# Kernel tuning notes

Hardware: AMD Instinct MI355X
Metric: run time of the kernel (lower is better)

## Reference

```python
import jax, jax.numpy as jnp
import numpy as np

K = 24            # patch_size (window)
D = 4             # dilation
C = 256           # dim
H = 8             # num_heads
N = 500000        # number of octree tokens at this depth (nnum_t)
BATCH_SIZE = 8
BLOCK = K * D
NA = int(np.ceil(N / BLOCK)) * BLOCK   # nnum_a (padded length)
PAD = NA - N
SCALE = (C // H) ** -0.5
MASK_VAL = -1000.0


def setup_inputs() -> dict:
    key = jax.random.key(0)
    k1, k2, k3, k4 = jax.random.split(key, 4)
    data = jax.random.normal(k1, (N, C), jnp.float32)
    qkv_w = jax.random.normal(k2, (3 * C, C), jnp.float32) * 0.02
    qkv_b = jnp.zeros((3 * C,), jnp.float32)
    proj_w = jax.random.normal(k3, (C, C), jnp.float32) * 0.02
    proj_b = jnp.zeros((C,), jnp.float32)
    batch_idx = jnp.sort(jax.random.randint(k4, (N,), 0, BATCH_SIZE, dtype=jnp.int32))
    return {"data": data, "qkv_w": qkv_w, "qkv_b": qkv_b,
            "proj_w": proj_w, "proj_b": proj_b, "batch_idx": batch_idx}


def _dilate_mask(batch_idx):
    # patch_partition of batch ids: pad with fill_value = batch_size
    b = jnp.concatenate([batch_idx, jnp.full((PAD,), BATCH_SIZE, jnp.int32)], axis=0)
    # dilate reshuffle: (-1, K, D) -> transpose -> (-1, K) windows
    b = b.reshape(-1, K, D).transpose(0, 2, 1).reshape(-1, K)
    diff = b[:, :, None] - b[:, None, :]           # [nw, K, K]
    return jnp.where(diff != 0, MASK_VAL, 0.0).astype(jnp.float32)


def reference(data, qkv_w, qkv_b, proj_w, proj_b, batch_idx):
    mask = _dilate_mask(batch_idx)                              # [nw, K, K]
    # patch_partition of features: pad with zeros
    x = jnp.concatenate([data, jnp.zeros((PAD, C), data.dtype)], axis=0)
    # dilation reshuffle: (-1, K, D, C) -> (-1, D, K, C) -> windows [nw, K, C]
    x = x.reshape(-1, K, D, C).transpose(0, 2, 1, 3).reshape(-1, K, C)
    qkv = (x @ qkv_w.T + qkv_b).reshape(-1, K, 3, H, C // H).transpose(2, 0, 3, 1, 4)
    q, k, v = qkv[0] * SCALE, qkv[1], qkv[2]                    # [nw, H, K, hd]
    attn = jnp.einsum('nhqd,nhkd->nhqk', q, k) + mask[:, None]  # [nw, H, K, K]
    attn = jax.nn.softmax(attn, axis=-1)
    out = jnp.einsum('nhqk,nhkd->nhqd', attn, v)
    out = out.transpose(0, 2, 1, 3).reshape(-1, C)              # merge heads
    # reverse dilation reshuffle, drop padding (patch_reverse)
    out = out.reshape(-1, D, K, C).transpose(0, 2, 1, 3).reshape(-1, C)[:N]
    return out @ proj_w.T + proj_b
```

## Files before the change

### kernel.cpp

```cpp
#include <hip/hip_runtime.h>


#define N_TOK 500000
#define NA    500064
#define MP    500096
#define MT    3907
#define MT8   3912
#define CDIM  256
#define KWIN  24
#define NWIN  20836
#define HEADS 8
#define SCALE_F 0.17677669529663689f

typedef __attribute__((ext_vector_type(8))) short bf16x8;
typedef __attribute__((ext_vector_type(4))) float f32x4;

__device__ __forceinline__ unsigned short f2b(float f) {
    unsigned int u = __float_as_uint(f);
    u += 0x7fffu + ((u >> 16) & 1u);
    return (unsigned short)(u >> 16);
}

#define GLOAD_LDS16(gsrc, ldst) \
    __builtin_amdgcn_global_load_lds((const __attribute__((address_space(1))) void*)(gsrc), \
                                     (__attribute__((address_space(3))) void*)(ldst), 16, 0, 0)


__global__ __launch_bounds__(256) void cvt_w_kernel(const float* __restrict__ src,
                                                    unsigned short* __restrict__ dst, int n8) {
    int i = blockIdx.x * 256 + threadIdx.x;
    if (i >= n8) return;
    float4 a = ((const float4*)src)[i * 2];
    float4 b = ((const float4*)src)[i * 2 + 1];
    uint4 o;
    o.x = (unsigned)f2b(a.x) | ((unsigned)f2b(a.y) << 16);
    o.y = (unsigned)f2b(a.z) | ((unsigned)f2b(a.w) << 16);
    o.z = (unsigned)f2b(b.x) | ((unsigned)f2b(b.y) << 16);
    o.w = (unsigned)f2b(b.z) | ((unsigned)f2b(b.w) << 16);
    ((uint4*)dst)[i] = o;
}


__global__ __launch_bounds__(256, 3) void qkv_gemm_kernel(const float* __restrict__ A32,
                                                          const unsigned short* __restrict__ Bt,
                                                          const float* __restrict__ bias,
                                                          unsigned short* __restrict__ out) {
    __shared__ unsigned short ldsA[128 * 64];
    __shared__ unsigned short ldsB[128 * 64];
    const int l = blockIdx.x;
    const int s = l >> 3;
    const int mtile = (l & 7) + 8 * (s / 6);
    const int ntile = s - (s / 6) * 6;
    if (mtile >= MT) return;

    const int tid  = threadIdx.x;
    const int lane = tid & 63;
    const int wv   = tid >> 6;
    const int wr   = wv >> 1, wc = wv & 1;

    f32x4 acc[4][4];
    #pragma unroll
    for (int i = 0; i < 4; ++i)
        #pragma unroll
        for (int j = 0; j < 4; ++j)
            #pragma unroll
            for (int r = 0; r < 4; ++r) acc[i][j][r] = 0.f;

    const char*  bbase = (const char*)(Bt + (size_t)ntile * 128 * CDIM);
    const int lrow8 = lane >> 3;
    const int lcolb_sw = (((lane & 7) ^ lrow8) << 4);
    const int arow  = tid >> 4;
    const int acol  = (tid & 15) * 4;
    const int awz   = (arow & 7) << 4;
    const int growb = mtile * 128;
    const bool full_tile = (growb + 128 <= N_TOK);
    char* ldsA_b = (char*)ldsA;
    const int lrow = lane & 15, lg = lane >> 4;
    const int swzr = (lrow & 7) << 4;

    for (int kt = 0; kt < 4; ++kt) {
        #pragma unroll
        for (int c = 0; c < 4; ++c) {
            int chunk = wv * 4 + c;
            int row = chunk * 8 + lrow8;
            GLOAD_LDS16(bbase + (size_t)row * 512 + kt * 128 + lcolb_sw, &ldsB[chunk * 512]);
        }
        float4 areg[8];
        if (full_tile) {
            #pragma unroll
            for (int i = 0; i < 8; ++i) {
                int row_g = growb + i * 16 + arow;
                areg[i] = *(const float4*)(A32 + (size_t)row_g * CDIM + kt * 64 + acol);
            }
        } else {
            #pragma unroll
            for (int i = 0; i < 8; ++i) {
                int row_g = growb + i * 16 + arow;
                int row_c = row_g < N_TOK ? row_g : (N_TOK - 1);
                areg[i] = *(const float4*)(A32 + (size_t)row_c * CDIM + kt * 64 + acol);
            }
            #pragma unroll
            for (int i = 0; i < 8; ++i)
                if (growb + i * 16 + arow >= N_TOK) areg[i] = make_float4(0.f, 0.f, 0.f, 0.f);
        }
        #pragma unroll
        for (int i = 0; i < 8; ++i) {
            float4 a = areg[i];
            uint2 o;
            o.x = (unsigned)f2b(a.x) | ((unsigned)f2b(a.y) << 16);
            o.y = (unsigned)f2b(a.z) | ((unsigned)f2b(a.w) << 16);
            *(uint2*)(ldsA_b + (i * 16 + arow) * 128 + (((tid & 15) * 8) ^ awz)) = o;
        }
        __syncthreads();
        #pragma unroll
        for (int ks = 0; ks < 2; ++ks) {
            const int kbyte = ks * 64 + lg * 16;
            bf16x8 af[4], bfr[4];
            #pragma unroll
            for (int i = 0; i < 4; ++i) {
                int ra = wr * 64 + i * 16 + lrow;
                int rb = wc * 64 + i * 16 + lrow;
                af[i]  = *(const bf16x8*)(ldsA_b + ra * 128 + (kbyte ^ swzr));
                bfr[i] = *(const bf16x8*)((const char*)ldsB + rb * 128 + (kbyte ^ swzr));
            }
            #pragma unroll
            for (int i = 0; i < 4; ++i)
                #pragma unroll
                for (int j = 0; j < 4; ++j)
                    acc[i][j] = __builtin_amdgcn_mfma_f32_16x16x32_bf16(af[i], bfr[j], acc[i][j], 0, 0, 0);
        }
        __syncthreads();
    }

    #pragma unroll
    for (int i = 0; i < 4; ++i) {
        int row0 = mtile * 128 + wr * 64 + i * 16 + lg * 4;
        #pragma unroll
        for (int j = 0; j < 4; ++j) {
            int col = ntile * 128 + wc * 64 + j * 16 + lrow;
            float bv = bias[col];
            #pragma unroll
            for (int r = 0; r < 4; ++r)
                out[(size_t)(row0 + r) * 768 + col] = f2b(acc[i][j][r] + bv);
        }
    }
}


__global__ __launch_bounds__(512, 2) void attn_proj_kernel(const unsigned short* __restrict__ qkv,
                                                           const int* __restrict__ batch_idx,
                                                           const unsigned short* __restrict__ wproj,
                                                           const float* __restrict__ pbias,
                                                           float* __restrict__ dout) {
    __shared__ unsigned short sP[8][32 * 64];
    __shared__ unsigned short sX[32 * 256];

    const int bid = blockIdx.x;
    const int xcd = bid & 7, sidx = bid >> 3;
    const int qch = NWIN >> 3, rch = NWIN & 7;
    const int w = (xcd < rch ? xcd * (qch + 1) : rch * (qch + 1) + (xcd - rch) * qch) + sidx;

    const int tid  = threadIdx.x;
    const int lane = tid & 63;
    const int h    = tid >> 6;
    const int gw = w >> 2, dd = w & 3;
    const int lrow = lane & 15, lg = lane >> 4;
    const int pbase = gw * 96 + dd;

    bf16x8 Qf[2], Kf[2];
    #pragma unroll
    for (int t = 0; t < 2; ++t) {
        size_t p = (size_t)(pbase + (t * 16 + lrow) * 4);
        const unsigned short* bp = qkv + p * 768 + h * 32 + lg * 8;
        Qf[t] = *(const bf16x8*)bp;
        Kf[t] = *(const bf16x8*)(bp + 256);
    }
    unsigned short v0[8], v1[8];
    #pragma unroll
    for (int j2 = 0; j2 < 8; ++j2) {
        size_t p = (size_t)(pbase + (lg * 8 + j2) * 4);
        const unsigned short* vp = qkv + p * 768 + 512 + h * 32 + lrow;
        v0[j2] = vp[0];
        v1[j2] = vp[16];
    }
    int bq[2];
    #pragma unroll
    for (int j = 0; j < 2; ++j) {
        int r = j * 16 + lrow;
        int p = pbase + r * 4;
        bq[j] = (r < KWIN && p < N_TOK) ? batch_idx[p] : -1;
    }
    int bk[2][4];
    #pragma unroll
    for (int i = 0; i < 2; ++i)
        #pragma unroll
        for (int rr = 0; rr < 4; ++rr) {
            int r = i * 16 + lg * 4 + rr;
            int p = pbase + r * 4;
            bk[i][rr] = (r < KWIN && p < N_TOK) ? batch_idx[p] : -2;
        }

    f32x4 accS[2][2];
    #pragma unroll
    for (int i = 0; i < 2; ++i)
        #pragma unroll
        for (int j = 0; j < 2; ++j)
            #pragma unroll
            for (int r = 0; r < 4; ++r) accS[i][j][r] = 0.f;
    #pragma unroll
    for (int i = 0; i < 2; ++i)
        #pragma unroll
        for (int j = 0; j < 2; ++j)
            accS[i][j] = __builtin_amdgcn_mfma_f32_16x16x32_bf16(Kf[i], Qf[j], accS[i][j], 0, 0, 0);

    float sv[2][2][4];
    float mx[2] = { -3.0e38f, -3.0e38f };
    #pragma unroll
    for (int i = 0; i < 2; ++i)
        #pragma unroll
        for (int j = 0; j < 2; ++j)
            #pragma unroll
            for (int rr = 0; rr < 4; ++rr) {
                float val = (bk[i][rr] == bq[j]) ? accS[i][j][rr] * SCALE_F : -1.0e9f;
                sv[i][j][rr] = val;
                mx[j] = fmaxf(mx[j], val);
            }
    mx[0] = fmaxf(mx[0], __shfl_xor(mx[0], 16)); mx[0] = fmaxf(mx[0], __shfl_xor(mx[0], 32));
    mx[1] = fmaxf(mx[1], __shfl_xor(mx[1], 16)); mx[1] = fmaxf(mx[1], __shfl_xor(mx[1], 32));
    float sm[2] = { 0.f, 0.f };
    #pragma unroll
    for (int i = 0; i < 2; ++i)
        #pragma unroll
        for (int j = 0; j < 2; ++j)
            #pragma unroll
            for (int rr = 0; rr < 4; ++rr) {
                float e = __expf(sv[i][j][rr] - mx[j]);
                sv[i][j][rr] = e;
                sm[j] += e;
            }
    sm[0] += __shfl_xor(sm[0], 16); sm[0] += __shfl_xor(sm[0], 32);
    sm[1] += __shfl_xor(sm[1], 16); sm[1] += __shfl_xor(sm[1], 32);
    float inv[2] = { 1.f / sm[0], 1.f / sm[1] };

    char* pb = (char*)sP[h];
    const int swz = (lrow & 7) << 4;
    #pragma unroll
    for (int j = 0; j < 2; ++j) {
        int q = j * 16 + lrow;
        #pragma unroll
        for (int i = 0; i < 2; ++i) {
            unsigned lo = (unsigned)f2b(sv[i][j][0] * inv[j]) | ((unsigned)f2b(sv[i][j][1] * inv[j]) << 16);
            unsigned hi = (unsigned)f2b(sv[i][j][2] * inv[j]) | ((unsigned)f2b(sv[i][j][3] * inv[j]) << 16);
            *(uint2*)(pb + q * 128 + ((i * 32 + lg * 8) ^ swz)) = make_uint2(lo, hi);
        }
    }
    bf16x8 AP[2];
    #pragma unroll
    for (int jj = 0; jj < 2; ++jj)
        AP[jj] = *(const bf16x8*)(pb + (jj * 16 + lrow) * 128 + ((lg * 16) ^ swz));

    union { bf16x8 v; unsigned short s[8]; } B0, B1;
    #pragma unroll
    for (int j2 = 0; j2 < 8; ++j2) { B0.s[j2] = v0[j2]; B1.s[j2] = v1[j2]; }
    f32x4 accO[2][2];
    #pragma unroll
    for (int i = 0; i < 2; ++i)
        #pragma unroll
        for (int j = 0; j < 2; ++j)
            #pragma unroll
            for (int r = 0; r < 4; ++r) accO[i][j][r] = 0.f;
    #pragma unroll
    for (int jj = 0; jj < 2; ++jj) {
        accO[jj][0] = __builtin_amdgcn_mfma_f32_16x16x32_bf16(AP[jj], B0.v, accO[jj][0], 0, 0, 0);
        accO[jj][1] = __builtin_amdgcn_mfma_f32_16x16x32_bf16(AP[jj], B1.v, accO[jj][1], 0, 0, 0);
    }

    char* xb = (char*)sX;
    #pragma unroll
    for (int jj = 0; jj < 2; ++jj)
        #pragma unroll
        for (int nd = 0; nd < 2; ++nd)
            #pragma unroll
            for (int rr = 0; rr < 4; ++rr) {
                int q = jj * 16 + lg * 4 + rr;
                int c = h * 32 + nd * 16 + lrow;
                *(unsigned short*)(xb + q * 512 + ((c * 2) ^ ((q & 15) << 4))) = f2b(accO[jj][nd][rr]);
            }

    bf16x8 WB[2][8];
    #pragma unroll
    for (int nt = 0; nt < 2; ++nt)
        #pragma unroll
        for (int k8 = 0; k8 < 8; ++k8)
            WB[nt][k8] = *(const bf16x8*)(wproj + (size_t)(h * 32 + nt * 16 + lrow) * 256 + k8 * 32 + lg * 8);

    __syncthreads();

    f32x4 acc2[2][2];
    #pragma unroll
    for (int mt = 0; mt < 2; ++mt)
        #pragma unroll
        for (int nt = 0; nt < 2; ++nt)
            #pragma unroll
            for (int r = 0; r < 4; ++r) acc2[mt][nt][r] = 0.f;
    #pragma unroll
    for (int k8 = 0; k8 < 8; ++k8) {
        bf16x8 aA[2];
        #pragma unroll
        for (int mt = 0; mt < 2; ++mt)
            aA[mt] = *(const bf16x8*)(xb + (mt * 16 + lrow) * 512 + ((k8 * 64 + lg * 16) ^ (lrow << 4)));
        #pragma unroll
        for (int mt = 0; mt < 2; ++mt)
            #pragma unroll
            for (int nt = 0; nt < 2; ++nt)
                acc2[mt][nt] = __builtin_amdgcn_mfma_f32_16x16x32_bf16(aA[mt], WB[nt][k8], acc2[mt][nt], 0, 0, 0);
    }

    #pragma unroll
    for (int nt = 0; nt < 2; ++nt) {
        int n = h * 32 + nt * 16 + lrow;
        float bv = pbias[n];
        #pragma unroll
        for (int mt = 0; mt < 2; ++mt)
            #pragma unroll
            for (int rr = 0; rr < 4; ++rr) {
                int q = mt * 16 + lg * 4 + rr;
                int p = pbase + q * 4;
                if (q < KWIN && p < N_TOK)
                    dout[(size_t)p * CDIM + n] = acc2[mt][nt][rr] + bv;
            }
    }
}


extern "C" void kernel_launch(void* const* d_in, const int* in_sizes, int n_in,
                              void* d_out, int out_size, void* d_ws, size_t ws_size,
                              hipStream_t stream) {
    const float* data    = (const float*)d_in[0];
    const float* qkv_w   = (const float*)d_in[1];
    const float* qkv_b   = (const float*)d_in[2];
    const float* proj_w  = (const float*)d_in[3];
    const float* proj_b  = (const float*)d_in[4];
    const int*   batch_i = (const int*)d_in[5];

    char* ws = (char*)d_ws;
    size_t off = 0;
    unsigned short* qkvB   = (unsigned short*)(ws + off); off += (size_t)MP * 768 * 2;
    unsigned short* wqkvB  = (unsigned short*)(ws + off); off += (size_t)768 * 256 * 2;
    unsigned short* wprojB = (unsigned short*)(ws + off); off += (size_t)256 * 256 * 2;
    if (ws_size < off) return;

    cvt_w_kernel<<<(768 * 256 / 8 + 255) / 256, 256, 0, stream>>>(qkv_w, wqkvB, 768 * 256 / 8);
    cvt_w_kernel<<<(256 * 256 / 8 + 255) / 256, 256, 0, stream>>>(proj_w, wprojB, 256 * 256 / 8);

    qkv_gemm_kernel<<<MT8 * 6, 256, 0, stream>>>(data, wqkvB, qkv_b, qkvB);
    attn_proj_kernel<<<NWIN, 512, 0, stream>>>(qkvB, batch_i, wprojB, proj_b, (float*)d_out);
}
```

Baseline: 1.005 ms.

## Process a full 96-token window group per block with LDS-staged QKV

Measured after the change: 954.9 us. 1.05x faster.

```diff
diff --git a/kernel.cpp b/kernel.cpp
--- a/kernel.cpp
+++ b/kernel.cpp
@@ -6,9 +6,9 @@
 #define MP    500096
 #define MT    3907
 #define MT8   3912
+#define NG    5209
 #define CDIM  256
 #define KWIN  24
-#define NWIN  20836
 #define HEADS 8
 #define SCALE_F 0.17677669529663689f
 
@@ -147,170 +147,199 @@
 }
 
 
-__global__ __launch_bounds__(512, 2) void attn_proj_kernel(const unsigned short* __restrict__ qkv,
+__global__ __launch_bounds__(512, 1) void attn_proj_kernel(const unsigned short* __restrict__ qkv,
                                                            const int* __restrict__ batch_idx,
                                                            const unsigned short* __restrict__ wproj,
                                                            const float* __restrict__ pbias,
                                                            float* __restrict__ dout) {
-    __shared__ unsigned short sP[8][32 * 64];
-    __shared__ unsigned short sX[32 * 256];
-
-    const int bid = blockIdx.x;
-    const int xcd = bid & 7, sidx = bid >> 3;
-    const int qch = NWIN >> 3, rch = NWIN & 7;
-    const int w = (xcd < rch ? xcd * (qch + 1) : rch * (qch + 1) + (xcd - rch) * qch) + sidx;
-
+    __shared__ __align__(16) unsigned char ldsx[162816];
+    const int g    = blockIdx.x;
     const int tid  = threadIdx.x;
     const int lane = tid & 63;
-    const int h    = tid >> 6;
-    const int gw = w >> 2, dd = w & 3;
+    const int wv   = tid >> 6;
     const int lrow = lane & 15, lg = lane >> 4;
-    const int pbase = gw * 96 + dd;
-
-    bf16x8 Qf[2], Kf[2];
-    #pragma unroll
-    for (int t = 0; t < 2; ++t) {
-        size_t p = (size_t)(pbase + (t * 16 + lrow) * 4);
-        const unsigned short* bp = qkv + p * 768 + h * 32 + lg * 8;
-        Qf[t] = *(const bf16x8*)bp;
-        Kf[t] = *(const bf16x8*)(bp + 256);
-    }
-    unsigned short v0[8], v1[8];
-    #pragma unroll
-    for (int j2 = 0; j2 < 8; ++j2) {
-        size_t p = (size_t)(pbase + (lg * 8 + j2) * 4);
-        const unsigned short* vp = qkv + p * 768 + 512 + h * 32 + lrow;
-        v0[j2] = vp[0];
-        v1[j2] = vp[16];
-    }
-    int bq[2];
-    #pragma unroll
-    for (int j = 0; j < 2; ++j) {
-        int r = j * 16 + lrow;
-        int p = pbase + r * 4;
-        bq[j] = (r < KWIN && p < N_TOK) ? batch_idx[p] : -1;
-    }
-    int bk[2][4];
-    #pragma unroll
-    for (int i = 0; i < 2; ++i)
-        #pragma unroll
-        for (int rr = 0; rr < 4; ++rr) {
-            int r = i * 16 + lg * 4 + rr;
-            int p = pbase + r * 4;
-            bk[i][rr] = (r < KWIN && p < N_TOK) ? batch_idx[p] : -2;
-        }
-
-    f32x4 accS[2][2];
-    #pragma unroll
-    for (int i = 0; i < 2; ++i)
-        #pragma unroll
-        for (int j = 0; j < 2; ++j)
-            #pragma unroll
-            for (int r = 0; r < 4; ++r) accS[i][j][r] = 0.f;
-    #pragma unroll
-    for (int i = 0; i < 2; ++i)
-        #pragma unroll
-        for (int j = 0; j < 2; ++j)
-            accS[i][j] = __builtin_amdgcn_mfma_f32_16x16x32_bf16(Kf[i], Qf[j], accS[i][j], 0, 0, 0);
-
-    float sv[2][2][4];
-    float mx[2] = { -3.0e38f, -3.0e38f };
-    #pragma unroll
-    for (int i = 0; i < 2; ++i)
-        #pragma unroll
-        for (int j = 0; j < 2; ++j)
+
+    const char* gbase = (const char*)qkv + (size_t)g * 147456;
+    #pragma unroll
+    for (int c = 0; c < 18; ++c) {
+        int s = c * 512 + tid;
+        int row = s / 96;
+        int c16 = s - row * 96;
+        int srcb = (c16 * 16) ^ (((row >> 2) & 7) << 4);
+        GLOAD_LDS16(gbase + row * 1536 + srcb, ldsx + (size_t)(c * 512 + wv * 64) * 16);
+    }
+    __syncthreads();
+
+    const char* X = (const char*)ldsx;
+    char* sPw = (char*)ldsx + 147456 + wv * 1920;
+    f32x4 accO4[4][2][2];
+
+    #pragma unroll
+    for (int tt = 0; tt < 4; ++tt) {
+        const int task = wv * 4 + tt;
+        const int dd = task >> 3, h = task & 7;
+
+        bf16x8 Qf[2], Kf[2];
+        #pragma unroll
+        for (int t = 0; t < 2; ++t) {
+            int q  = t * 16 + lrow;
+            int rq = (q < KWIN) ? q * 4 + dd : dd;
+            int sz = ((rq >> 2) & 7) << 4;
+            Qf[t] = *(const bf16x8*)(X + rq * 1536 + ((h * 64 + lg * 16) ^ sz));
+            Kf[t] = *(const bf16x8*)(X + rq * 1536 + ((512 + h * 64 + lg * 16) ^ sz));
+        }
+        unsigned short v0[8], v1[8];
+        #pragma unroll
+        for (int j2 = 0; j2 < 8; ++j2) {
+            int k  = lg * 8 + j2;
+            int rv = (k < KWIN) ? k * 4 + dd : dd;
+            int sz = ((rv >> 2) & 7) << 4;
+            v0[j2] = *(const unsigned short*)(X + rv * 1536 + ((1024 + h * 64 + lrow * 2) ^ sz));
+            v1[j2] = *(const unsigned short*)(X + rv * 1536 + ((1024 + h * 64 + 32 + lrow * 2) ^ sz));
+        }
+        int bq[2];
+        #pragma unroll
+        for (int j = 0; j < 2; ++j) {
+            int q = j * 16 + lrow;
+            int p = g * 96 + q * 4 + dd;
+            bq[j] = (q < KWIN && p < N_TOK) ? batch_idx[p] : -1;
+        }
+        int bk[2][4];
+        #pragma unroll
+        for (int i = 0; i < 2; ++i)
             #pragma unroll
             for (int rr = 0; rr < 4; ++rr) {
-                float val = (bk[i][rr] == bq[j]) ? accS[i][j][rr] * SCALE_F : -1.0e9f;
-                sv[i][j][rr] = val;
-                mx[j] = fmaxf(mx[j], val);
-            }
-    mx[0] = fmaxf(mx[0], __shfl_xor(mx[0], 16)); mx[0] = fmaxf(mx[0], __shfl_xor(mx[0], 32));
-    mx[1] = fmaxf(mx[1], __shfl_xor(mx[1], 16)); mx[1] = fmaxf(mx[1], __shfl_xor(mx[1], 32));
-    float sm[2] = { 0.f, 0.f };
-    #pragma unroll
-    for (int i = 0; i < 2; ++i)
-        #pragma unroll
-        for (int j = 0; j < 2; ++j)
-            #pragma unroll
-            for (int rr = 0; rr < 4; ++rr) {
-                float e = __expf(sv[i][j][rr] - mx[j]);
-                sv[i][j][rr] = e;
-                sm[j] += e;
-            }
-    sm[0] += __shfl_xor(sm[0], 16); sm[0] += __shfl_xor(sm[0], 32);
-    sm[1] += __shfl_xor(sm[1], 16); sm[1] += __shfl_xor(sm[1], 32);
-    float inv[2] = { 1.f / sm[0], 1.f / sm[1] };
-
-    char* pb = (char*)sP[h];
-    const int swz = (lrow & 7) << 4;
-    #pragma unroll
-    for (int j = 0; j < 2; ++j) {
-        int q = j * 16 + lrow;
-        #pragma unroll
-        for (int i = 0; i < 2; ++i) {
-            unsigned lo = (unsigned)f2b(sv[i][j][0] * inv[j]) | ((unsigned)f2b(sv[i][j][1] * inv[j]) << 16);
-            unsigned hi = (unsigned)f2b(sv[i][j][2] * inv[j]) | ((unsigned)f2b(sv[i][j][3] * inv[j]) << 16);
-            *(uint2*)(pb + q * 128 + ((i * 32 + lg * 8) ^ swz)) = make_uint2(lo, hi);
-        }
-    }
-    bf16x8 AP[2];
-    #pragma unroll
-    for (int jj = 0; jj < 2; ++jj)
-        AP[jj] = *(const bf16x8*)(pb + (jj * 16 + lrow) * 128 + ((lg * 16) ^ swz));
-
-    union { bf16x8 v; unsigned short s[8]; } B0, B1;
-    #pragma unroll
-    for (int j2 = 0; j2 < 8; ++j2) { B0.s[j2] = v0[j2]; B1.s[j2] = v1[j2]; }
-    f32x4 accO[2][2];
-    #pragma unroll
-    for (int i = 0; i < 2; ++i)
-        #pragma unroll
-        for (int j = 0; j < 2; ++j)
-            #pragma unroll
-            for (int r = 0; r < 4; ++r) accO[i][j][r] = 0.f;
-    #pragma unroll
-    for (int jj = 0; jj < 2; ++jj) {
-        accO[jj][0] = __builtin_amdgcn_mfma_f32_16x16x32_bf16(AP[jj], B0.v, accO[jj][0], 0, 0, 0);
-        accO[jj][1] = __builtin_amdgcn_mfma_f32_16x16x32_bf16(AP[jj], B1.v, accO[jj][1], 0, 0, 0);
-    }
-
-    char* xb = (char*)sX;
-    #pragma unroll
-    for (int jj = 0; jj < 2; ++jj)
-        #pragma unroll
-        for (int nd = 0; nd < 2; ++nd)
-            #pragma unroll
-            for (int rr = 0; rr < 4; ++rr) {
-                int q = jj * 16 + lg * 4 + rr;
-                int c = h * 32 + nd * 16 + lrow;
-                *(unsigned short*)(xb + q * 512 + ((c * 2) ^ ((q & 15) << 4))) = f2b(accO[jj][nd][rr]);
-            }
+                int k = i * 16 + lg * 4 + rr;
+                int p = g * 96 + k * 4 + dd;
+                bk[i][rr] = (k < KWIN && p < N_TOK) ? batch_idx[p] : -2;
+            }
+
+        f32x4 accS[2][2];
+        #pragma unroll
+        for (int i = 0; i < 2; ++i)
+            #pragma unroll
+            for (int j = 0; j < 2; ++j)
+                #pragma unroll
+                for (int r = 0; r < 4; ++r) accS[i][j][r] = 0.f;
+        #pragma unroll
+        for (int i = 0; i < 2; ++i)
+            #pragma unroll
+            for (int j = 0; j < 2; ++j)
+                accS[i][j] = __builtin_amdgcn_mfma_f32_16x16x32_bf16(Kf[i], Qf[j], accS[i][j], 0, 0, 0);
+
+        float sv[2][2][4];
+        float mx[2] = { -3.0e38f, -3.0e38f };
+        #pragma unroll
+        for (int i = 0; i < 2; ++i)
+            #pragma unroll
+            for (int j = 0; j < 2; ++j)
+                #pragma unroll
+                for (int rr = 0; rr < 4; ++rr) {
+                    float val = (bk[i][rr] == bq[j]) ? accS[i][j][rr] * SCALE_F : -1.0e9f;
+                    sv[i][j][rr] = val;
+                    mx[j] = fmaxf(mx[j], val);
+                }
+        mx[0] = fmaxf(mx[0], __shfl_xor(mx[0], 16)); mx[0] = fmaxf(mx[0], __shfl_xor(mx[0], 32));
+        mx[1] = fmaxf(mx[1], __shfl_xor(mx[1], 16)); mx[1] = fmaxf(mx[1], __shfl_xor(mx[1], 32));
+        float sm[2] = { 0.f, 0.f };
+        #pragma unroll
+        for (int i = 0; i < 2; ++i)
+            #pragma unroll
+            for (int j = 0; j < 2; ++j)
+                #pragma unroll
+                for (int rr = 0; rr < 4; ++rr) {
+                    float e = __expf(sv[i][j][rr] - mx[j]);
+                    sv[i][j][rr] = e;
+                    sm[j] += e;
+                }
+        sm[0] += __shfl_xor(sm[0], 16); sm[0] += __shfl_xor(sm[0], 32);
+        sm[1] += __shfl_xor(sm[1], 16); sm[1] += __shfl_xor(sm[1], 32);
+        float inv[2] = { 1.f / sm[0], 1.f / sm[1] };
+
+        #pragma unroll
+        for (int j = 0; j < 2; ++j) {
+            if (j == 0 || lrow < 8) {
+                int q = j * 16 + lrow;
+                #pragma unroll
+                for (int i = 0; i < 2; ++i) {
+                    unsigned lo = (unsigned)f2b(sv[i][j][0] * inv[j]) | ((unsigned)f2b(sv[i][j][1] * inv[j]) << 16);
+                    unsigned hi = (unsigned)f2b(sv[i][j][2] * inv[j]) | ((unsigned)f2b(sv[i][j][3] * inv[j]) << 16);
+                    *(uint2*)(sPw + q * 80 + i * 32 + lg * 8) = make_uint2(lo, hi);
+                }
+            }
+        }
+        bf16x8 AP[2];
+        #pragma unroll
+        for (int jj = 0; jj < 2; ++jj) {
+            int qr = jj * 16 + lrow;
+            if (qr > 23) qr = 23;
+            AP[jj] = *(const bf16x8*)(sPw + qr * 80 + lg * 16);
+        }
+
+        union { bf16x8 v; unsigned short s[8]; } B0, B1;
+        #pragma unroll
+        for (int j2 = 0; j2 < 8; ++j2) { B0.s[j2] = v0[j2]; B1.s[j2] = v1[j2]; }
+        #pragma unroll
+        for (int jj = 0; jj < 2; ++jj)
+            #pragma unroll
+            for (int nd = 0; nd < 2; ++nd)
+                #pragma unroll
+                for (int r = 0; r < 4; ++r) accO4[tt][jj][nd][r] = 0.f;
+        #pragma unroll
+        for (int jj = 0; jj < 2; ++jj) {
+            accO4[tt][jj][0] = __builtin_amdgcn_mfma_f32_16x16x32_bf16(AP[jj], B0.v, accO4[tt][jj][0], 0, 0, 0);
+            accO4[tt][jj][1] = __builtin_amdgcn_mfma_f32_16x16x32_bf16(AP[jj], B1.v, accO4[tt][jj][1], 0, 0, 0);
+        }
+    }
+
+    __syncthreads();
+
+    char* xw = (char*)ldsx;
+    #pragma unroll
+    for (int tt = 0; tt < 4; ++tt) {
+        const int task = wv * 4 + tt;
+        const int dd = task >> 3, h = task & 7;
+        #pragma unroll
+        for (int jj = 0; jj < 2; ++jj)
+            #pragma unroll
+            for (int nd = 0; nd < 2; ++nd)
+                #pragma unroll
+                for (int rr = 0; rr < 4; ++rr) {
+                    int q = jj * 16 + lg * 4 + rr;
+                    if (q < KWIN) {
+                        int r  = q * 4 + dd;
+                        int cb = h * 64 + nd * 32 + lrow * 2;
+                        *(unsigned short*)(xw + r * 512 + (cb ^ ((r & 7) << 4))) = f2b(accO4[tt][jj][nd][rr]);
+                    }
+                }
+    }
 
     bf16x8 WB[2][8];
     #pragma unroll
     for (int nt = 0; nt < 2; ++nt)
         #pragma unroll
         for (int k8 = 0; k8 < 8; ++k8)
-            WB[nt][k8] = *(const bf16x8*)(wproj + (size_t)(h * 32 + nt * 16 + lrow) * 256 + k8 * 32 + lg * 8);
+            WB[nt][k8] = *(const bf16x8*)(wproj + (size_t)(wv * 32 + nt * 16 + lrow) * 256 + k8 * 32 + lg * 8);
 
     __syncthreads();
 
-    f32x4 acc2[2][2];
-    #pragma unroll
-    for (int mt = 0; mt < 2; ++mt)
+    f32x4 acc2[6][2];
+    #pragma unroll
+    for (int mt = 0; mt < 6; ++mt)
         #pragma unroll
         for (int nt = 0; nt < 2; ++nt)
             #pragma unroll
             for (int r = 0; r < 4; ++r) acc2[mt][nt][r] = 0.f;
     #pragma unroll
     for (int k8 = 0; k8 < 8; ++k8) {
-        bf16x8 aA[2];
-        #pragma unroll
-        for (int mt = 0; mt < 2; ++mt)
-            aA[mt] = *(const bf16x8*)(xb + (mt * 16 + lrow) * 512 + ((k8 * 64 + lg * 16) ^ (lrow << 4)));
-        #pragma unroll
-        for (int mt = 0; mt < 2; ++mt)
+        bf16x8 aA[6];
+        #pragma unroll
+        for (int mt = 0; mt < 6; ++mt) {
+            int ra = mt * 16 + lrow;
+            aA[mt] = *(const bf16x8*)(X + ra * 512 + ((k8 * 64 + lg * 16) ^ ((ra & 7) << 4)));
+        }
+        #pragma unroll
+        for (int mt = 0; mt < 6; ++mt)
             #pragma unroll
             for (int nt = 0; nt < 2; ++nt)
                 acc2[mt][nt] = __builtin_amdgcn_mfma_f32_16x16x32_bf16(aA[mt], WB[nt][k8], acc2[mt][nt], 0, 0, 0);
@@ -318,15 +347,15 @@
 
     #pragma unroll
     for (int nt = 0; nt < 2; ++nt) {
-        int n = h * 32 + nt * 16 + lrow;
+        int n = wv * 32 + nt * 16 + lrow;
         float bv = pbias[n];
         #pragma unroll
-        for (int mt = 0; mt < 2; ++mt)
+        for (int mt = 0; mt < 6; ++mt)
             #pragma unroll
             for (int rr = 0; rr < 4; ++rr) {
-                int q = mt * 16 + lg * 4 + rr;
-                int p = pbase + q * 4;
-                if (q < KWIN && p < N_TOK)
+                int r = mt * 16 + lg * 4 + rr;
+                int p = g * 96 + r;
+                if (p < N_TOK)
                     dout[(size_t)p * CDIM + n] = acc2[mt][nt][rr] + bv;
             }
     }
@@ -354,5 +383,5 @@
     cvt_w_kernel<<<(256 * 256 / 8 + 255) / 256, 256, 0, stream>>>(proj_w, wprojB, 256 * 256 / 8);
 
     qkv_gemm_kernel<<<MT8 * 6, 256, 0, stream>>>(data, wqkvB, qkv_b, qkvB);
-    attn_proj_kernel<<<NWIN, 512, 0, stream>>>(qkvB, batch_i, wprojB, proj_b, (float*)d_out);
-}
+    attn_proj_kernel<<<NG, 512, 0, stream>>>(qkvB, batch_i, wprojB, proj_b, (float*)d_out);
+}
```
